# Performance work log

Measured on AMD Instinct MI355X. Metric: run time of the kernel, lower is better.

The kernel has to match this reference:

```python
import jax, jax.numpy as jnp
import numpy as np


@jax.custom_vjp
def binarize(w):
    # BNN-style sign binarization: forward sign(w), backward straight-through (identity)
    return jnp.sign(w)


def _binarize_fwd(w):
    return jnp.sign(w), None


def _binarize_bwd(_, g):
    return (g,)


binarize.defvjp(_binarize_fwd, _binarize_bwd)


def setup_inputs() -> dict:
    key = jax.random.key(0)
    kx, kw = jax.random.split(key)
    N, IN, OUT = 4096, 4096, 4096
    x = jax.random.normal(kx, (N, IN), dtype=jnp.float32)
    # xavier_normal init: std = sqrt(2 / (fan_in + fan_out))
    std = (2.0 / (IN + OUT)) ** 0.5
    W = jax.random.normal(kw, (OUT, IN), dtype=jnp.float32) * std
    b = jnp.zeros((OUT,), dtype=jnp.float32)
    return {"x": x, "W": W, "b": b}


def reference(x, W, b):
    wb = binarize(W)                      # [OUT, IN] in {-1, 0, +1}
    return x @ wb.T + b                   # [N, OUT]
```

## Files before the change

kernel.cpp:

```cpp
#include <hip/hip_runtime.h>
#include <hip/hip_bf16.h>
#include <stdint.h>

typedef __attribute__((ext_vector_type(8))) short short8;
typedef __attribute__((ext_vector_type(8))) unsigned short ushort8;
typedef __attribute__((ext_vector_type(4))) float f32x4;
typedef unsigned short ushort_t;


__device__ inline unsigned short f2bf_rne(float f) {
    union { float f; unsigned int u; } v; v.f = f;
    unsigned int u = v.u;
    unsigned int r = u + 0x7FFFu + ((u >> 16) & 1u);
    return (unsigned short)(r >> 16);
}

__global__ __launch_bounds__(256) void cvt_x_kernel(const float* __restrict__ in,
                                                    unsigned short* __restrict__ out,
                                                    int n8) {
    int i = blockIdx.x * blockDim.x + threadIdx.x;
    if (i >= n8) return;
    const float4* p = reinterpret_cast<const float4*>(in) + (size_t)i * 2;
    float4 a = p[0];
    float4 b = p[1];
    ushort8 o;
    o[0] = f2bf_rne(a.x); o[1] = f2bf_rne(a.y); o[2] = f2bf_rne(a.z); o[3] = f2bf_rne(a.w);
    o[4] = f2bf_rne(b.x); o[5] = f2bf_rne(b.y); o[6] = f2bf_rne(b.z); o[7] = f2bf_rne(b.w);
    *reinterpret_cast<ushort8*>(out + (size_t)i * 8) = o;
}

__device__ inline unsigned short signbf(float f) {
    return (f > 0.0f) ? (unsigned short)0x3F80u
         : (f < 0.0f) ? (unsigned short)0xBF80u
                      : (unsigned short)0u;
}

__global__ __launch_bounds__(256) void cvt_w_kernel(const float* __restrict__ in,
                                                    unsigned short* __restrict__ out,
                                                    int n8) {
    int i = blockIdx.x * blockDim.x + threadIdx.x;
    if (i >= n8) return;
    const float4* p = reinterpret_cast<const float4*>(in) + (size_t)i * 2;
    float4 a = p[0];
    float4 b = p[1];
    ushort8 o;
    o[0] = signbf(a.x); o[1] = signbf(a.y); o[2] = signbf(a.z); o[3] = signbf(a.w);
    o[4] = signbf(b.x); o[5] = signbf(b.y); o[6] = signbf(b.z); o[7] = signbf(b.w);
    *reinterpret_cast<ushort8*>(out + (size_t)i * 8) = o;
}


#define BM 256
#define BN 256
#define BK 64

__device__ __forceinline__ void gload_lds16(const void* g, void* l) {
    __builtin_amdgcn_global_load_lds(
        (const __attribute__((address_space(1))) unsigned int*)g,
        (__attribute__((address_space(3))) unsigned int*)l,
        16, 0, 0);
}

__device__ __forceinline__ void phase_barrier() {
    __builtin_amdgcn_sched_barrier(0);
    __builtin_amdgcn_s_barrier();
    __builtin_amdgcn_sched_barrier(0);
}

__device__ __forceinline__ void stage_tile(
    const ushort_t* __restrict__ A, const ushort_t* __restrict__ B,
    ushort_t* ldsA, ushort_t* ldsB,
    int brow, int bcol, int kbase, int K,
    int wid, int srow, int scol)
{
#pragma unroll
    for (int h = 0; h < 2; ++h)
#pragma unroll
        for (int r = 0; r < 2; ++r) {
            const int rowoff = h * 128 + r * 64 + wid * 8;
            const ushort_t* ga = A + (size_t)(brow + rowoff + srow) * K + kbase + scol;
            gload_lds16(ga, ldsA + rowoff * 64);
            const ushort_t* gb = B + (size_t)(bcol + rowoff + srow) * K + kbase + scol;
            gload_lds16(gb, ldsB + rowoff * 64);
        }
}

__global__ __launch_bounds__(512, 2) void gemm8_bt_bias(
    const ushort_t* __restrict__ A,
    const ushort_t* __restrict__ B,
    const float* __restrict__ bias,
    float* __restrict__ C,
    int M, int N, int K, int tn_n)
{
    extern __shared__ ushort_t lds[];

    const int tid  = threadIdx.x;
    const int wid  = tid >> 6;
    const int lane = tid & 63;
    const int wr = wid >> 2;
    const int wc = wid & 3;

    unsigned nwg = gridDim.x, orig = blockIdx.x;
    unsigned qd = nwg >> 3, rm = nwg & 7u;
    unsigned xcd = orig & 7u, sub = orig >> 3;
    unsigned id = (xcd < rm ? xcd * (qd + 1) : rm * (qd + 1) + (xcd - rm) * qd) + sub;
    const int tm = (int)(id / (unsigned)tn_n);
    const int tn = (int)(id % (unsigned)tn_n);
    const int brow = tm * BM;
    const int bcol = tn * BN;

    const int nt = K / BK;

    const int srow = lane >> 3;
    const int scol = ((lane & 7) ^ srow) << 3;

    const int r15 = lane & 15;
    const int hi2 = lane >> 4;
    const int l7  = lane & 7;
    const int sK0 = ((hi2) ^ l7) * 8;
    const int sK1 = ((4 + hi2) ^ l7) * 8;
    const int bRow = (wc & 1) * 64;

    f32x4 acc[8][4];
#pragma unroll
    for (int m = 0; m < 8; ++m)
#pragma unroll
        for (int n = 0; n < 4; ++n)
            acc[m][n] = (f32x4){0.f, 0.f, 0.f, 0.f};

    stage_tile(A, B, lds, lds + 32768, brow, bcol, 0, K, wid, srow, scol);
    __syncthreads();

    short8 aF[2][4], bF[2][4];

#pragma unroll 2
    for (int t = 0; t < nt; ++t) {
        const int cur = t & 1;
        const ushort_t* aC = lds + cur * 16384 + wr * 8192;
        const ushort_t* bC = lds + 32768 + cur * 16384 + (wc >> 1) * 8192;

        if (t + 1 < nt) {
            const int nxt = cur ^ 1;
            stage_tile(A, B, lds + nxt * 16384, lds + 32768 + nxt * 16384,
                       brow, bcol, (t + 1) * BK, K, wid, srow, scol);
        }

#pragma unroll
        for (int i = 0; i < 4; ++i) {
            aF[0][i] = *reinterpret_cast<const short8*>(aC + (i * 16 + r15) * 64 + sK0);
            aF[1][i] = *reinterpret_cast<const short8*>(aC + (i * 16 + r15) * 64 + sK1);
        }
#pragma unroll
        for (int n = 0; n < 2; ++n) {
            bF[0][n] = *reinterpret_cast<const short8*>(bC + (bRow + n * 16 + r15) * 64 + sK0);
            bF[1][n] = *reinterpret_cast<const short8*>(bC + (bRow + n * 16 + r15) * 64 + sK1);
        }
        phase_barrier();
        __builtin_amdgcn_s_setprio(1);
#pragma unroll
        for (int i = 0; i < 4; ++i)
#pragma unroll
            for (int j = 0; j < 2; ++j) {
                f32x4 c = acc[i][j];
                c = __builtin_amdgcn_mfma_f32_16x16x32_bf16(aF[0][i], bF[0][j], c, 0, 0, 0);
                c = __builtin_amdgcn_mfma_f32_16x16x32_bf16(aF[1][i], bF[1][j], c, 0, 0, 0);
                acc[i][j] = c;
            }
        __builtin_amdgcn_s_setprio(0);
        phase_barrier();

#pragma unroll
        for (int n = 2; n < 4; ++n) {
            bF[0][n] = *reinterpret_cast<const short8*>(bC + (bRow + n * 16 + r15) * 64 + sK0);
            bF[1][n] = *reinterpret_cast<const short8*>(bC + (bRow + n * 16 + r15) * 64 + sK1);
        }
        phase_barrier();
        __builtin_amdgcn_s_setprio(1);
#pragma unroll
        for (int i = 0; i < 4; ++i)
#pragma unroll
            for (int j = 2; j < 4; ++j) {
                f32x4 c = acc[i][j];
                c = __builtin_amdgcn_mfma_f32_16x16x32_bf16(aF[0][i], bF[0][j], c, 0, 0, 0);
                c = __builtin_amdgcn_mfma_f32_16x16x32_bf16(aF[1][i], bF[1][j], c, 0, 0, 0);
                acc[i][j] = c;
            }
        __builtin_amdgcn_s_setprio(0);
        phase_barrier();

#pragma unroll
        for (int i = 0; i < 4; ++i) {
            aF[0][i] = *reinterpret_cast<const short8*>(aC + ((4 + i) * 16 + r15) * 64 + sK0);
            aF[1][i] = *reinterpret_cast<const short8*>(aC + ((4 + i) * 16 + r15) * 64 + sK1);
        }
        phase_barrier();
        __builtin_amdgcn_s_setprio(1);
#pragma unroll
        for (int i = 0; i < 4; ++i)
#pragma unroll
            for (int j = 0; j < 2; ++j) {
                f32x4 c = acc[4 + i][j];
                c = __builtin_amdgcn_mfma_f32_16x16x32_bf16(aF[0][i], bF[0][j], c, 0, 0, 0);
                c = __builtin_amdgcn_mfma_f32_16x16x32_bf16(aF[1][i], bF[1][j], c, 0, 0, 0);
                acc[4 + i][j] = c;
            }
        __builtin_amdgcn_s_setprio(0);
        phase_barrier();

        __builtin_amdgcn_s_setprio(1);
#pragma unroll
        for (int i = 0; i < 4; ++i)
#pragma unroll
            for (int j = 2; j < 4; ++j) {
                f32x4 c = acc[4 + i][j];
                c = __builtin_amdgcn_mfma_f32_16x16x32_bf16(aF[0][i], bF[0][j], c, 0, 0, 0);
                c = __builtin_amdgcn_mfma_f32_16x16x32_bf16(aF[1][i], bF[1][j], c, 0, 0, 0);
                acc[4 + i][j] = c;
            }
        __builtin_amdgcn_s_setprio(0);

        __syncthreads();
    }

#pragma unroll
    for (int n = 0; n < 4; ++n) {
        const int col = bcol + wc * 64 + n * 16 + r15;
        const float bv = bias[col];
#pragma unroll
        for (int m = 0; m < 8; ++m) {
            const int row0 = brow + wr * 128 + m * 16 + hi2 * 4;
#pragma unroll
            for (int j = 0; j < 4; ++j) {
                C[(size_t)(row0 + j) * N + col] = acc[m][n][j] + bv;
            }
        }
    }
}


extern "C" void kernel_launch(void* const* d_in, const int* in_sizes, int n_in,
                              void* d_out, int out_size, void* d_ws, size_t ws_size,
                              hipStream_t stream) {
    const float* x  = (const float*)d_in[0];
    const float* W  = (const float*)d_in[1];
    const float* bv = (const float*)d_in[2];
    float* out = (float*)d_out;

    const int OUT = in_sizes[2];
    const int IN  = in_sizes[1] / OUT;
    const int M   = in_sizes[0] / IN;

    unsigned short* xb = (unsigned short*)d_ws;
    unsigned short* wb = xb + (size_t)M * IN;

    {
        const int n8 = (M * IN) / 8;
        cvt_x_kernel<<<(n8 + 255) / 256, 256, 0, stream>>>(x, xb, n8);
    }
    {
        const int n8 = (OUT * IN) / 8;
        cvt_w_kernel<<<(n8 + 255) / 256, 256, 0, stream>>>(W, wb, n8);
    }

    const int tn_n = OUT / BN;
    const int tm_n = M / BM;
    const int nblk = tn_n * tm_n;
    (void)hipFuncSetAttribute((const void*)gemm8_bt_bias,
                              hipFuncAttributeMaxDynamicSharedMemorySize, 131072);
    gemm8_bt_bias<<<nblk, 512, 131072, stream>>>(xb, wb, bv, out, M, OUT, IN, tn_n);
}
```

Before: 290.4 us.

## Fuse conversion kernels and use partial vmcnt waits in the GEMM pipeline

The two fp32-to-bf16 conversion kernels are merged into one grid-stride kernel, which saves a launch. In the GEMM, the prefetch loads are reordered so that the A and B halves needed first are issued first. The full __syncthreads waits are replaced with s_waitcnt vmcnt(N) plus s_barrier, so later loads can stay in flight while MFMAs run. The last iteration now prefetches a dummy k=0 tile unconditionally, which keeps the vmcnt counts uniform at the cost of one redundant tile load.

```diff
diff --git a/kernel.cpp b/kernel.cpp
--- a/kernel.cpp
+++ b/kernel.cpp
@@ -8,45 +8,43 @@
 typedef unsigned short ushort_t;
 
 
-__device__ inline unsigned short f2bf_rne(float f) {
+__device__ __forceinline__ unsigned short f2bf_rne(float f) {
     union { float f; unsigned int u; } v; v.f = f;
     unsigned int u = v.u;
     unsigned int r = u + 0x7FFFu + ((u >> 16) & 1u);
     return (unsigned short)(r >> 16);
 }
 
-__global__ __launch_bounds__(256) void cvt_x_kernel(const float* __restrict__ in,
-                                                    unsigned short* __restrict__ out,
-                                                    int n8) {
-    int i = blockIdx.x * blockDim.x + threadIdx.x;
-    if (i >= n8) return;
-    const float4* p = reinterpret_cast<const float4*>(in) + (size_t)i * 2;
-    float4 a = p[0];
-    float4 b = p[1];
-    ushort8 o;
-    o[0] = f2bf_rne(a.x); o[1] = f2bf_rne(a.y); o[2] = f2bf_rne(a.z); o[3] = f2bf_rne(a.w);
-    o[4] = f2bf_rne(b.x); o[5] = f2bf_rne(b.y); o[6] = f2bf_rne(b.z); o[7] = f2bf_rne(b.w);
-    *reinterpret_cast<ushort8*>(out + (size_t)i * 8) = o;
-}
-
-__device__ inline unsigned short signbf(float f) {
+__device__ __forceinline__ unsigned short signbf(float f) {
     return (f > 0.0f) ? (unsigned short)0x3F80u
          : (f < 0.0f) ? (unsigned short)0xBF80u
                       : (unsigned short)0u;
 }
 
-__global__ __launch_bounds__(256) void cvt_w_kernel(const float* __restrict__ in,
-                                                    unsigned short* __restrict__ out,
-                                                    int n8) {
-    int i = blockIdx.x * blockDim.x + threadIdx.x;
-    if (i >= n8) return;
-    const float4* p = reinterpret_cast<const float4*>(in) + (size_t)i * 2;
-    float4 a = p[0];
-    float4 b = p[1];
-    ushort8 o;
-    o[0] = signbf(a.x); o[1] = signbf(a.y); o[2] = signbf(a.z); o[3] = signbf(a.w);
-    o[4] = signbf(b.x); o[5] = signbf(b.y); o[6] = signbf(b.z); o[7] = signbf(b.w);
-    *reinterpret_cast<ushort8*>(out + (size_t)i * 8) = o;
+__global__ __launch_bounds__(256) void cvt_fused(
+    const float* __restrict__ x, const float* __restrict__ W,
+    ushort_t* __restrict__ xb, ushort_t* __restrict__ wb,
+    int n8x, int n8total)
+{
+    const int stride = gridDim.x * 256;
+    for (int i = blockIdx.x * 256 + threadIdx.x; i < n8total; i += stride) {
+        const bool isx = i < n8x;
+        const float* src = isx ? x : W;
+        ushort_t* dst    = isx ? xb : wb;
+        const int j      = isx ? i : i - n8x;
+        const float4* p = reinterpret_cast<const float4*>(src) + (size_t)j * 2;
+        float4 a = p[0];
+        float4 b = p[1];
+        ushort8 o;
+        if (isx) {
+            o[0] = f2bf_rne(a.x); o[1] = f2bf_rne(a.y); o[2] = f2bf_rne(a.z); o[3] = f2bf_rne(a.w);
+            o[4] = f2bf_rne(b.x); o[5] = f2bf_rne(b.y); o[6] = f2bf_rne(b.z); o[7] = f2bf_rne(b.w);
+        } else {
+            o[0] = signbf(a.x); o[1] = signbf(a.y); o[2] = signbf(a.z); o[3] = signbf(a.w);
+            o[4] = signbf(b.x); o[5] = signbf(b.y); o[6] = signbf(b.z); o[7] = signbf(b.w);
+        }
+        *reinterpret_cast<ushort8*>(dst + (size_t)j * 8) = o;
+    }
 }
 
 
@@ -63,6 +61,20 @@
 
 __device__ __forceinline__ void phase_barrier() {
     __builtin_amdgcn_sched_barrier(0);
+    __builtin_amdgcn_s_barrier();
+    __builtin_amdgcn_sched_barrier(0);
+}
+
+__device__ __forceinline__ void bar_vm8() {
+    __builtin_amdgcn_sched_barrier(0);
+    asm volatile("s_waitcnt vmcnt(8)" ::: "memory");
+    __builtin_amdgcn_s_barrier();
+    __builtin_amdgcn_sched_barrier(0);
+}
+
+__device__ __forceinline__ void bar_vm2() {
+    __builtin_amdgcn_sched_barrier(0);
+    asm volatile("s_waitcnt vmcnt(2)" ::: "memory");
     __builtin_amdgcn_s_barrier();
     __builtin_amdgcn_sched_barrier(0);
 }
@@ -73,16 +85,15 @@
     int brow, int bcol, int kbase, int K,
     int wid, int srow, int scol)
 {
-#pragma unroll
-    for (int h = 0; h < 2; ++h)
-#pragma unroll
-        for (int r = 0; r < 2; ++r) {
-            const int rowoff = h * 128 + r * 64 + wid * 8;
-            const ushort_t* ga = A + (size_t)(brow + rowoff + srow) * K + kbase + scol;
-            gload_lds16(ga, ldsA + rowoff * 64);
-            const ushort_t* gb = B + (size_t)(bcol + rowoff + srow) * K + kbase + scol;
-            gload_lds16(gb, ldsB + rowoff * 64);
-        }
+    const int ro0 = wid * 8;
+    gload_lds16(A + (size_t)(brow + 0   + ro0 + srow) * K + kbase + scol, ldsA + (0   + ro0) * 64);
+    gload_lds16(A + (size_t)(brow + 128 + ro0 + srow) * K + kbase + scol, ldsA + (128 + ro0) * 64);
+    gload_lds16(B + (size_t)(bcol + 0   + ro0 + srow) * K + kbase + scol, ldsB + (0   + ro0) * 64);
+    gload_lds16(B + (size_t)(bcol + 128 + ro0 + srow) * K + kbase + scol, ldsB + (128 + ro0) * 64);
+    gload_lds16(B + (size_t)(bcol + 64  + ro0 + srow) * K + kbase + scol, ldsB + (64  + ro0) * 64);
+    gload_lds16(B + (size_t)(bcol + 192 + ro0 + srow) * K + kbase + scol, ldsB + (192 + ro0) * 64);
+    gload_lds16(A + (size_t)(brow + 64  + ro0 + srow) * K + kbase + scol, ldsA + (64  + ro0) * 64);
+    gload_lds16(A + (size_t)(brow + 192 + ro0 + srow) * K + kbase + scol, ldsA + (192 + ro0) * 64);
 }
 
 __global__ __launch_bounds__(512, 2) void gemm8_bt_bias(
@@ -129,21 +140,19 @@
             acc[m][n] = (f32x4){0.f, 0.f, 0.f, 0.f};
 
     stage_tile(A, B, lds, lds + 32768, brow, bcol, 0, K, wid, srow, scol);
-    __syncthreads();
+    bar_vm2();
 
     short8 aF[2][4], bF[2][4];
 
-#pragma unroll 2
     for (int t = 0; t < nt; ++t) {
         const int cur = t & 1;
+        const int nxt = cur ^ 1;
         const ushort_t* aC = lds + cur * 16384 + wr * 8192;
         const ushort_t* bC = lds + 32768 + cur * 16384 + (wc >> 1) * 8192;
-
-        if (t + 1 < nt) {
-            const int nxt = cur ^ 1;
-            stage_tile(A, B, lds + nxt * 16384, lds + 32768 + nxt * 16384,
-                       brow, bcol, (t + 1) * BK, K, wid, srow, scol);
-        }
+        const int kn = (t == nt - 1) ? 0 : (t + 1) * BK;
+
+        stage_tile(A, B, lds + nxt * 16384, lds + 32768 + nxt * 16384,
+                   brow, bcol, kn, K, wid, srow, scol);
 
 #pragma unroll
         for (int i = 0; i < 4; ++i) {
@@ -186,7 +195,7 @@
                 acc[i][j] = c;
             }
         __builtin_amdgcn_s_setprio(0);
-        phase_barrier();
+        bar_vm8();
 
 #pragma unroll
         for (int i = 0; i < 4; ++i) {
@@ -219,7 +228,7 @@
             }
         __builtin_amdgcn_s_setprio(0);
 
-        __syncthreads();
+        bar_vm2();
     }
 
 #pragma unroll
@@ -253,14 +262,9 @@
     unsigned short* xb = (unsigned short*)d_ws;
     unsigned short* wb = xb + (size_t)M * IN;
 
-    {
-        const int n8 = (M * IN) / 8;
-        cvt_x_kernel<<<(n8 + 255) / 256, 256, 0, stream>>>(x, xb, n8);
-    }
-    {
-        const int n8 = (OUT * IN) / 8;
-        cvt_w_kernel<<<(n8 + 255) / 256, 256, 0, stream>>>(W, wb, n8);
-    }
+    const int n8x = (M * IN) / 8;
+    const int n8w = (OUT * IN) / 8;
+    cvt_fused<<<2048, 256, 0, stream>>>(x, W, xb, wb, n8x, n8x + n8w);
 
     const int tn_n = OUT / BN;
     const int tm_n = M / BM;
```

After: 293.0 us. No clear change (+0.9%).
